# Kernel optimization log

Measured on AMD Instinct MI355X. Metric: run time of the kernel, lower is better.

## Reference

```python
import jax, jax.numpy as jnp
import numpy as np

N = 50000
E = 1600000


def _gcn_norm(edge_index, num_nodes):
    # PyG gcn_norm with add_self_loops=True, edge_weight=1:
    # append self loops, deg = in-degree over dst (col), norm = d_src^-1/2 * d_dst^-1/2
    loops = jnp.arange(num_nodes, dtype=edge_index.dtype)
    src = jnp.concatenate([edge_index[0], loops])
    dst = jnp.concatenate([edge_index[1], loops])
    deg = jax.ops.segment_sum(jnp.ones_like(dst, dtype=jnp.float32), dst,
                              num_segments=num_nodes)
    dinv = jnp.where(deg > 0, jax.lax.rsqrt(deg), 0.0)
    norm = dinv[src] * dinv[dst]  # [E+N]
    return src, dst, norm


def _gcn_layer(x, W, b, src, dst, norm, num_nodes):
    h = x @ W                                  # [N, out]
    msg = h[src] * norm[:, None]               # gather + scale, [E+N, out]
    out = jax.ops.segment_sum(msg, dst, num_segments=num_nodes)
    return out + b


def setup_inputs() -> dict:
    key = jax.random.key(0)
    ks = jax.random.split(key, 10)
    d_in, d_h, d_out = 128, 128, 64
    s = lambda d: 1.0 / np.sqrt(d)
    return {
        "x": jax.random.normal(ks[0], (N, d_in), dtype=jnp.float32),
        "edge_index": jax.random.randint(ks[1], (2, E), 0, N, dtype=jnp.int64),
        "W1": jax.random.normal(ks[2], (d_in, d_h), dtype=jnp.float32) * s(d_in),
        "b1": jnp.zeros((d_h,), dtype=jnp.float32),
        "W2": jax.random.normal(ks[3], (d_h, d_h), dtype=jnp.float32) * s(d_h),
        "b2": jnp.zeros((d_h,), dtype=jnp.float32),
        "W3": jax.random.normal(ks[4], (d_h, d_h), dtype=jnp.float32) * s(d_h),
        "b3": jnp.zeros((d_h,), dtype=jnp.float32),
        "W4": jax.random.normal(ks[5], (d_h, d_out), dtype=jnp.float32) * s(d_h),
        "b4": jnp.zeros((d_out,), dtype=jnp.float32),
    }


def reference(x, edge_index, W1, b1, W2, b2, W3, b3, W4, b4):
    src, dst, norm = _gcn_norm(edge_index, N)
    h = jax.nn.relu(_gcn_layer(x, W1, b1, src, dst, norm, N))
    h = jax.nn.relu(_gcn_layer(h, W2, b2, src, dst, norm, N))
    h = jax.nn.relu(_gcn_layer(h, W3, b3, src, dst, norm, N))
    h = _gcn_layer(h, W4, b4, src, dst, norm, N)
    return h
```

## Files before the change

kernel.cpp:

```cpp
#include <hip/hip_runtime.h>
#include <hip/hip_fp16.h>

constexpr int K_DIM = 128;

typedef short bf16x8 __attribute__((ext_vector_type(8)));
typedef float f32x4 __attribute__((ext_vector_type(4)));
typedef unsigned uint4e __attribute__((ext_vector_type(4)));

#define GLOAD16(g, l) __builtin_amdgcn_global_load_lds( \
    (const __attribute__((address_space(1))) void*)(g), \
    (__attribute__((address_space(3))) void*)(l), 16, 0, 0)

__device__ __forceinline__ unsigned short f2bf(float f) {
  unsigned u = __float_as_uint(f);
  u += 0x7fff + ((u >> 16) & 1);
  return (unsigned short)(u >> 16);
}
__device__ __forceinline__ float bf2f(unsigned short s) {
  return __uint_as_float(((unsigned)s) << 16);
}

__global__ void zerob_k(int* __restrict__ bcount, int NBr) {
  int t = threadIdx.x;
  if (t < NBr) bcount[t] = 0;
}

__global__ __launch_bounds__(256) void bcount_k(const int* __restrict__ dst, int E,
    int* __restrict__ bcount, int NBr) {
  __shared__ int h[256];
  const int tid = threadIdx.x;
  h[tid] = 0;
  __syncthreads();
  for (int t = blockIdx.x * 256 + tid; t < E; t += gridDim.x * 256)
    atomicAdd(&h[dst[t] >> 8], 1);
  __syncthreads();
  if (tid < NBr && h[tid]) atomicAdd(&bcount[tid], h[tid]);
}

__global__ __launch_bounds__(256) void bscan_k(const int* __restrict__ bcount,
    int* __restrict__ bstart, int* __restrict__ bcursor, int NBr) {
  __shared__ int sh[256];
  const int t = threadIdx.x;
  sh[t] = (t < NBr) ? bcount[t] : 0;
  __syncthreads();
  for (int off = 1; off < 256; off <<= 1) {
    int w = (t >= off) ? sh[t - off] : 0;
    __syncthreads();
    sh[t] += w;
    __syncthreads();
  }
  if (t < NBr) {
    int ex = t ? sh[t - 1] : 0;
    bstart[t] = ex;
    bcursor[t] = ex;
  }
  if (t == NBr - 1) bstart[NBr] = sh[t];
}

__global__ __launch_bounds__(256) void bscatter_k(const int* __restrict__ ei, int E,
    int* __restrict__ bcursor, unsigned* __restrict__ brec, int NBr) {
  __shared__ int h[256];
  __shared__ int base[256];
  const int tid = threadIdx.x;
  h[tid] = 0;
  __syncthreads();
  const int chunk = (E + gridDim.x - 1) / gridDim.x;
  const int s = blockIdx.x * chunk;
  const int e = min(E, s + chunk);
  for (int t = s + tid; t < e; t += 256) atomicAdd(&h[ei[E + t] >> 8], 1);
  __syncthreads();
  if (tid < NBr && h[tid]) base[tid] = atomicAdd(&bcursor[tid], h[tid]);
  __syncthreads();
  for (int t = s + tid; t < e; t += 256) {
    int src = ei[t];
    int d = ei[E + t];
    int bk = d >> 8;
    int p = atomicAdd(&base[bk], 1);
    brec[p] = ((unsigned)src << 8) | (unsigned)(d & 255);
  }
}

__global__ __launch_bounds__(256) void bcsr_k(const unsigned* __restrict__ brec,
    const int* __restrict__ bstart, int n, int E,
    int* __restrict__ rowptr, int* __restrict__ colidx, float* __restrict__ dinv) {
  __shared__ int s_deg[256];
  __shared__ int s_cur[256];
  __shared__ int s_lrp[257];
  const int b = blockIdx.x, tid = threadIdx.x;
  const int node0 = b << 8;
  const int LC = min(256, n - node0);
  const int rs = bstart[b], cnt = bstart[b + 1] - rs;

  s_deg[tid] = (tid < LC) ? 1 : 0;
  __syncthreads();
  for (int i = tid; i < cnt; i += 256) atomicAdd(&s_deg[brec[rs + i] & 255], 1);
  __syncthreads();
  s_cur[tid] = s_deg[tid];
  __syncthreads();
  for (int off = 1; off < 256; off <<= 1) {
    int w = (tid >= off) ? s_cur[tid - off] : 0;
    __syncthreads();
    s_cur[tid] += w;
    __syncthreads();
  }
  s_lrp[tid + 1] = s_cur[tid];
  if (tid == 0) s_lrp[0] = 0;
  __syncthreads();

  const int gbase = rs + node0;
  if (tid < LC) {
    int p = s_lrp[tid];
    colidx[gbase + p] = node0 + tid;
    s_cur[tid] = p + 1;
    rowptr[node0 + tid] = gbase + p;
    dinv[node0 + tid] = rsqrtf((float)(s_lrp[tid + 1] - p));
  }
  __syncthreads();
  for (int i = tid; i < cnt; i += 256) {
    unsigned r = brec[rs + i];
    int p = atomicAdd(&s_cur[r & 255], 1);
    colidx[gbase + p] = (int)(r >> 8);
  }
  if (b == (int)gridDim.x - 1 && tid == 0) rowptr[n] = E + n;
}

__global__ __launch_bounds__(256) void split_k(const float* __restrict__ x,
    unsigned* __restrict__ zh, unsigned* __restrict__ zl, long total4) {
  long t = (long)blockIdx.x * 256 + threadIdx.x;
  if (t >= total4) return;
  float4 v = reinterpret_cast<const float4*>(x)[t];
  unsigned short hx = f2bf(v.x), hy = f2bf(v.y), hz = f2bf(v.z), hw = f2bf(v.w);
  unsigned short lx = f2bf(v.x - bf2f(hx)), ly = f2bf(v.y - bf2f(hy));
  unsigned short lz = f2bf(v.z - bf2f(hz)), lw = f2bf(v.w - bf2f(hw));
  reinterpret_cast<uint2*>(zh)[t] = make_uint2((unsigned)hx | ((unsigned)hy << 16),
                                               (unsigned)hz | ((unsigned)hw << 16));
  reinterpret_cast<uint2*>(zl)[t] = make_uint2((unsigned)lx | ((unsigned)ly << 16),
                                               (unsigned)lz | ((unsigned)lw << 16));
}

__global__ __launch_bounds__(256) void wprep_k(
    const float* __restrict__ W1, const float* __restrict__ W2,
    const float* __restrict__ W3, const float* __restrict__ W4,
    unsigned short* __restrict__ wth, unsigned short* __restrict__ wtl) {
  int id = blockIdx.x * 256 + threadIdx.x;
  if (id >= 57344) return;
  const float* W;
  int nout, base, rem;
  if (id < 49152) {
    int l = id / 16384;
    W = (l == 0) ? W1 : (l == 1) ? W2 : W3;
    nout = 128;
    base = l * 16384;
    rem = id - base;
  } else {
    W = W4;
    nout = 64;
    base = 49152;
    rem = id - base;
  }
  int k = rem / nout, c = rem % nout;
  float w = W[k * nout + c];
  unsigned short hi = f2bf(w);
  unsigned short lo = f2bf(w - bf2f(hi));
  wth[base + c * 128 + k] = hi;
  wtl[base + c * 128 + k] = lo;
}

template<int NOUT>
__global__ __launch_bounds__(256) void gemm_mfma_k(
    const unsigned short* __restrict__ Zh, const unsigned short* __restrict__ Zl,
    const unsigned short* __restrict__ Wh, const unsigned short* __restrict__ Wl,
    const float* __restrict__ dinv, __half* __restrict__ H, int n) {
  constexpr int NT = NOUT / 16;
  __shared__ unsigned short Ah[64][32];
  __shared__ unsigned short Al[64][32];
  __shared__ unsigned short Bh[NOUT][32];
  __shared__ unsigned short Bl[NOUT][32];
  const int tid = threadIdx.x;
  const int lane = tid & 63;
  const int w = tid >> 6;
  const int r16 = lane & 15;
  const int kb = lane >> 4;
  const int row0 = blockIdx.x * 64;

  f32x4 acc[NT];
  #pragma unroll
  for (int t = 0; t < NT; ++t)
    #pragma unroll
    for (int q = 0; q < 4; ++q) acc[t][q] = 0.f;

  char* AhB = (char*)&Ah[0][0];
  char* AlB = (char*)&Al[0][0];
  char* BhB = (char*)&Bh[0][0];
  char* BlB = (char*)&Bl[0][0];

  for (int kc = 0; kc < 128; kc += 32) {
    __syncthreads();
    {
      int rc = row0 + (tid >> 2); rc = (rc < n) ? rc : (n - 1);
      const unsigned short* gh = Zh + (size_t)rc * 128 + kc + (tid & 3) * 8;
      const unsigned short* gl = Zl + (size_t)rc * 128 + kc + (tid & 3) * 8;
      GLOAD16(gh, AhB + w * 1024);
      GLOAD16(gl, AlB + w * 1024);
    }
    {
      const unsigned short* gh = Wh + (size_t)(tid >> 2) * 128 + kc + (tid & 3) * 8;
      const unsigned short* gl = Wl + (size_t)(tid >> 2) * 128 + kc + (tid & 3) * 8;
      GLOAD16(gh, BhB + w * 1024);
      GLOAD16(gl, BlB + w * 1024);
      if constexpr (NOUT == 128) {
        int i1 = tid + 256;
        const unsigned short* gh1 = Wh + (size_t)(i1 >> 2) * 128 + kc + (i1 & 3) * 8;
        const unsigned short* gl1 = Wl + (size_t)(i1 >> 2) * 128 + kc + (i1 & 3) * 8;
        GLOAD16(gh1, BhB + 4096 + w * 1024);
        GLOAD16(gl1, BlB + 4096 + w * 1024);
      }
    }
    __syncthreads();

    bf16x8 ah = *(const bf16x8*)&Ah[w * 16 + r16][kb * 8];
    bf16x8 al = *(const bf16x8*)&Al[w * 16 + r16][kb * 8];
    #pragma unroll
    for (int t = 0; t < NT; ++t) {
      bf16x8 bh = *(const bf16x8*)&Bh[t * 16 + r16][kb * 8];
      bf16x8 bl = *(const bf16x8*)&Bl[t * 16 + r16][kb * 8];
      acc[t] = __builtin_amdgcn_mfma_f32_16x16x32_bf16(ah, bh, acc[t], 0, 0, 0);
      acc[t] = __builtin_amdgcn_mfma_f32_16x16x32_bf16(ah, bl, acc[t], 0, 0, 0);
      acc[t] = __builtin_amdgcn_mfma_f32_16x16x32_bf16(al, bh, acc[t], 0, 0, 0);
    }
  }

  #pragma unroll
  for (int q = 0; q < 4; ++q) {
    int grow = row0 + w * 16 + kb * 4 + q;
    if (grow < n) {
      float dsc = dinv[grow];
      #pragma unroll
      for (int t = 0; t < NT; ++t)
        H[(size_t)grow * NOUT + t * 16 + r16] = __float2half(dsc * acc[t][q]);
    }
  }
}

__global__ __launch_bounds__(256) void agg128_k(const __half* __restrict__ H,
    const int* __restrict__ rowptr, const int* __restrict__ colidx,
    const float* __restrict__ dinv, const float* __restrict__ bias,
    unsigned* __restrict__ Zh, unsigned* __restrict__ Zl, int n) {
  const int wave = threadIdx.x >> 6;
  const int lane = threadIdx.x & 63;
  const int node = blockIdx.x * 4 + wave;
  if (node >= n) return;
  const int s = rowptr[node], e = rowptr[node + 1];
  const __half2* H2 = reinterpret_cast<const __half2*>(H);

  float ax = 0.f, ay = 0.f;
  for (int base = s; base < e; base += 64) {
    int m = e - base;
    int c = __builtin_nontemporal_load(&colidx[base + ((lane < m) ? lane : 0)]);
    int kmax = (m < 64) ? m : 64;
    int k = 0;
    for (; k + 7 < kmax; k += 8) {
      int cc[8];
      float2 hh[8];
      #pragma unroll
      for (int u = 0; u < 8; ++u) cc[u] = __shfl(c, k + u);
      #pragma unroll
      for (int u = 0; u < 8; ++u) hh[u] = __half22float2(H2[(size_t)cc[u] * 64 + lane]);
      #pragma unroll
      for (int u = 0; u < 8; ++u) { ax += hh[u].x; ay += hh[u].y; }
    }
    for (; k < kmax; ++k) {
      int ck = __shfl(c, k);
      float2 h = __half22float2(H2[(size_t)ck * 64 + lane]);
      ax += h.x;
      ay += h.y;
    }
  }
  float d = dinv[node];
  float2 b2 = reinterpret_cast<const float2*>(bias)[lane];
  float ox = fmaxf(fmaf(d, ax, b2.x), 0.f);
  float oy = fmaxf(fmaf(d, ay, b2.y), 0.f);
  unsigned short hx = f2bf(ox), hy = f2bf(oy);
  unsigned short lx = f2bf(ox - bf2f(hx)), ly = f2bf(oy - bf2f(hy));
  unsigned vh = (unsigned)hx | ((unsigned)hy << 16);
  unsigned vl = (unsigned)lx | ((unsigned)ly << 16);
  __builtin_nontemporal_store(vh, &Zh[(size_t)node * 64 + lane]);
  __builtin_nontemporal_store(vl, &Zl[(size_t)node * 64 + lane]);
}

__global__ __launch_bounds__(256) void agg64_k(const __half* __restrict__ H,
    const int* __restrict__ rowptr, const int* __restrict__ colidx,
    const float* __restrict__ dinv, const float* __restrict__ bias,
    float* __restrict__ out, int n) {
  const int wave = threadIdx.x >> 6;
  const int lane = threadIdx.x & 63;
  const int node = blockIdx.x * 4 + wave;
  if (node >= n) return;
  const int s = rowptr[node], e = rowptr[node + 1];

  float a0 = 0.f;
  for (int base = s; base < e; base += 64) {
    int m = e - base;
    int c = __builtin_nontemporal_load(&colidx[base + ((lane < m) ? lane : 0)]);
    int kmax = (m < 64) ? m : 64;
    int k = 0;
    for (; k + 7 < kmax; k += 8) {
      int cc[8];
      float hh[8];
      #pragma unroll
      for (int u = 0; u < 8; ++u) cc[u] = __shfl(c, k + u);
      #pragma unroll
      for (int u = 0; u < 8; ++u) hh[u] = __half2float(H[(size_t)cc[u] * 64 + lane]);
      #pragma unroll
      for (int u = 0; u < 8; ++u) a0 += hh[u];
    }
    for (; k < kmax; ++k) {
      int ck = __shfl(c, k);
      a0 += __half2float(H[(size_t)ck * 64 + lane]);
    }
  }
  float o = fmaf(dinv[node], a0, bias[lane]);
  __builtin_nontemporal_store(o, &out[(size_t)node * 64 + lane]);
}

extern "C" void kernel_launch(void* const* d_in, const int* in_sizes, int n_in,
                              void* d_out, int out_size, void* d_ws, size_t ws_size,
                              hipStream_t stream) {
  const int n = in_sizes[0] / K_DIM;
  const int E = in_sizes[1] / 2;
  const int NBr = (n + 255) >> 8;

  const float* x  = (const float*)d_in[0];
  const int*   ei = (const int*)d_in[1];
  const float* W1 = (const float*)d_in[2];
  const float* b1 = (const float*)d_in[3];
  const float* W2 = (const float*)d_in[4];
  const float* b2 = (const float*)d_in[5];
  const float* W3 = (const float*)d_in[6];
  const float* b3 = (const float*)d_in[7];
  const float* W4 = (const float*)d_in[8];
  const float* b4 = (const float*)d_in[9];
  float* out = (float*)d_out;

  char* ws = (char*)d_ws;
  size_t off = 0;
  auto alloc = [&](size_t bytes) -> void* {
    void* p = ws + off;
    off += (bytes + 255) & ~(size_t)255;
    return p;
  };
  int*      bcount  = (int*)     alloc(256 * 4);
  int*      bstart  = (int*)     alloc(257 * 4);
  int*      bcursor = (int*)     alloc(256 * 4);
  unsigned* brec    = (unsigned*)alloc((size_t)E * 4);
  int*      rowptr  = (int*)     alloc((size_t)(n + 1) * 4);
  int*      colidx  = (int*)     alloc((size_t)(E + n) * 4);
  float*    dinv    = (float*)   alloc((size_t)n * 4);
  unsigned short* Zh = (unsigned short*)alloc((size_t)n * 128 * 2);
  unsigned short* Zl = (unsigned short*)alloc((size_t)n * 128 * 2);
  __half*   hH      = (__half*)  alloc((size_t)n * 128 * 2);
  unsigned short* wth = (unsigned short*)alloc((size_t)57344 * 2);
  unsigned short* wtl = (unsigned short*)alloc((size_t)57344 * 2);

  zerob_k<<<1, 256, 0, stream>>>(bcount, NBr);
  bcount_k<<<512, 256, 0, stream>>>(ei + E, E, bcount, NBr);
  bscan_k<<<1, 256, 0, stream>>>(bcount, bstart, bcursor, NBr);
  bscatter_k<<<256, 256, 0, stream>>>(ei, E, bcursor, brec, NBr);
  bcsr_k<<<NBr, 256, 0, stream>>>(brec, bstart, n, E, rowptr, colidx, dinv);

  const long total4 = (long)n * 32;
  split_k<<<(int)((total4 + 255) / 256), 256, 0, stream>>>(x, (unsigned*)Zh, (unsigned*)Zl, total4);
  wprep_k<<<224, 256, 0, stream>>>(W1, W2, W3, W4, wth, wtl);

  const int gb = (n + 63) / 64;
  const int ab = (n + 3) / 4;

  gemm_mfma_k<128><<<gb, 256, 0, stream>>>(Zh, Zl, wth, wtl, dinv, hH, n);
  agg128_k<<<ab, 256, 0, stream>>>(hH, rowptr, colidx, dinv, b1, (unsigned*)Zh, (unsigned*)Zl, n);
  gemm_mfma_k<128><<<gb, 256, 0, stream>>>(Zh, Zl, wth + 16384, wtl + 16384, dinv, hH, n);
  agg128_k<<<ab, 256, 0, stream>>>(hH, rowptr, colidx, dinv, b2, (unsigned*)Zh, (unsigned*)Zl, n);
  gemm_mfma_k<128><<<gb, 256, 0, stream>>>(Zh, Zl, wth + 32768, wtl + 32768, dinv, hH, n);
  agg128_k<<<ab, 256, 0, stream>>>(hH, rowptr, colidx, dinv, b3, (unsigned*)Zh, (unsigned*)Zl, n);
  gemm_mfma_k<64><<<gb, 256, 0, stream>>>(Zh, Zl, wth + 49152, wtl + 49152, dinv, hH, n);
  agg64_k<<<ab, 256, 0, stream>>>(hH, rowptr, colidx, dinv, b4, out, n);
}
```

Measured before the change: 324.0 us.

## Split hidden features into column halves and restructure GEMM with register-held weights

The GEMM now keeps the W tiles in registers, loads the full 64x128 A tile into swizzled LDS once, and has each wave compute a 32-row by half-column block. For 128-wide layers it writes H as two column-major halves of 64 features. Aggregation for those layers runs as two passes, one per half, with each half-wave gathering 32 half2 values per edge, two edges at a time. The aim is a smaller gather working set per pass for better L2 hit rates, plus fewer LDS round trips and syncs in the GEMM. The cost is double the CSR traversal and launches, more register pressure, and a cross-half-wave reduction.

New measurement: 409.6 us. +26.4%, slower.

```diff
diff --git a/kernel.cpp b/kernel.cpp
--- a/kernel.cpp
+++ b/kernel.cpp
@@ -5,7 +5,6 @@
 
 typedef short bf16x8 __attribute__((ext_vector_type(8)));
 typedef float f32x4 __attribute__((ext_vector_type(4)));
-typedef unsigned uint4e __attribute__((ext_vector_type(4)));
 
 #define GLOAD16(g, l) __builtin_amdgcn_global_load_lds( \
     (const __attribute__((address_space(1))) void*)(g), \
@@ -167,91 +166,107 @@
 }
 
 template<int NOUT>
-__global__ __launch_bounds__(256) void gemm_mfma_k(
+__global__ __launch_bounds__(256, 2) void gemm_mfma_k(
     const unsigned short* __restrict__ Zh, const unsigned short* __restrict__ Zl,
     const unsigned short* __restrict__ Wh, const unsigned short* __restrict__ Wl,
     const float* __restrict__ dinv, __half* __restrict__ H, int n) {
-  constexpr int NT = NOUT / 16;
-  __shared__ unsigned short Ah[64][32];
-  __shared__ unsigned short Al[64][32];
-  __shared__ unsigned short Bh[NOUT][32];
-  __shared__ unsigned short Bl[NOUT][32];
+  constexpr int CT = NOUT / 32;
+  __shared__ unsigned short Ah[64 * 128];
+  __shared__ unsigned short Al[64 * 128];
   const int tid = threadIdx.x;
   const int lane = tid & 63;
   const int w = tid >> 6;
   const int r16 = lane & 15;
   const int kb = lane >> 4;
   const int row0 = blockIdx.x * 64;
-
-  f32x4 acc[NT];
+  const int rbase = (w & 1) * 32;
+  const int cb = (w >> 1) * (NOUT / 2);
+
+  bf16x8 bh[CT][4], bl[CT][4];
   #pragma unroll
-  for (int t = 0; t < NT; ++t)
+  for (int t = 0; t < CT; ++t)
     #pragma unroll
-    for (int q = 0; q < 4; ++q) acc[t][q] = 0.f;
-
-  char* AhB = (char*)&Ah[0][0];
-  char* AlB = (char*)&Al[0][0];
-  char* BhB = (char*)&Bh[0][0];
-  char* BlB = (char*)&Bl[0][0];
-
-  for (int kc = 0; kc < 128; kc += 32) {
-    __syncthreads();
-    {
-      int rc = row0 + (tid >> 2); rc = (rc < n) ? rc : (n - 1);
-      const unsigned short* gh = Zh + (size_t)rc * 128 + kc + (tid & 3) * 8;
-      const unsigned short* gl = Zl + (size_t)rc * 128 + kc + (tid & 3) * 8;
-      GLOAD16(gh, AhB + w * 1024);
-      GLOAD16(gl, AlB + w * 1024);
-    }
-    {
-      const unsigned short* gh = Wh + (size_t)(tid >> 2) * 128 + kc + (tid & 3) * 8;
-      const unsigned short* gl = Wl + (size_t)(tid >> 2) * 128 + kc + (tid & 3) * 8;
-      GLOAD16(gh, BhB + w * 1024);
-      GLOAD16(gl, BlB + w * 1024);
-      if constexpr (NOUT == 128) {
-        int i1 = tid + 256;
-        const unsigned short* gh1 = Wh + (size_t)(i1 >> 2) * 128 + kc + (i1 & 3) * 8;
-        const unsigned short* gl1 = Wl + (size_t)(i1 >> 2) * 128 + kc + (i1 & 3) * 8;
-        GLOAD16(gh1, BhB + 4096 + w * 1024);
-        GLOAD16(gl1, BlB + 4096 + w * 1024);
+    for (int kc = 0; kc < 4; ++kc) {
+      size_t boff = (size_t)(cb + t * 16 + r16) * 128 + kc * 32 + kb * 8;
+      bh[t][kc] = *(const bf16x8*)&Wh[boff];
+      bl[t][kc] = *(const bf16x8*)&Wl[boff];
+    }
+
+  char* AhB = (char*)Ah;
+  char* AlB = (char*)Al;
+  #pragma unroll
+  for (int it = 0; it < 4; ++it) {
+    int i = it * 256 + tid;
+    int r = i >> 4;
+    int k2 = (i & 15) ^ (r & 7);
+    int rc = row0 + r; rc = (rc < n) ? rc : (n - 1);
+    GLOAD16(Zh + (size_t)rc * 128 + k2 * 8, AhB + it * 4096 + w * 1024);
+    GLOAD16(Zl + (size_t)rc * 128 + k2 * 8, AlB + it * 4096 + w * 1024);
+  }
+  __syncthreads();
+
+  f32x4 acc[2][CT];
+  #pragma unroll
+  for (int rf = 0; rf < 2; ++rf)
+    #pragma unroll
+    for (int t = 0; t < CT; ++t)
+      #pragma unroll
+      for (int q = 0; q < 4; ++q) acc[rf][t][q] = 0.f;
+
+  const int r0 = rbase + r16;
+  const int r1 = rbase + 16 + r16;
+  const int sw = r16 & 7;
+  #pragma unroll
+  for (int kc = 0; kc < 4; ++kc) {
+    int k2s = (kc * 4 + kb) ^ sw;
+    bf16x8 ah0 = *(const bf16x8*)(AhB + r0 * 256 + k2s * 16);
+    bf16x8 al0 = *(const bf16x8*)(AlB + r0 * 256 + k2s * 16);
+    bf16x8 ah1 = *(const bf16x8*)(AhB + r1 * 256 + k2s * 16);
+    bf16x8 al1 = *(const bf16x8*)(AlB + r1 * 256 + k2s * 16);
+    #pragma unroll
+    for (int t = 0; t < CT; ++t) {
+      acc[0][t] = __builtin_amdgcn_mfma_f32_16x16x32_bf16(ah0, bh[t][kc], acc[0][t], 0, 0, 0);
+      acc[0][t] = __builtin_amdgcn_mfma_f32_16x16x32_bf16(ah0, bl[t][kc], acc[0][t], 0, 0, 0);
+      acc[0][t] = __builtin_amdgcn_mfma_f32_16x16x32_bf16(al0, bh[t][kc], acc[0][t], 0, 0, 0);
+      acc[1][t] = __builtin_amdgcn_mfma_f32_16x16x32_bf16(ah1, bh[t][kc], acc[1][t], 0, 0, 0);
+      acc[1][t] = __builtin_amdgcn_mfma_f32_16x16x32_bf16(ah1, bl[t][kc], acc[1][t], 0, 0, 0);
+      acc[1][t] = __builtin_amdgcn_mfma_f32_16x16x32_bf16(al1, bh[t][kc], acc[1][t], 0, 0, 0);
+    }
+  }
+
+  #pragma unroll
+  for (int rf = 0; rf < 2; ++rf)
+    #pragma unroll
+    for (int q = 0; q < 4; ++q) {
+      int grow = row0 + rbase + rf * 16 + kb * 4 + q;
+      if (grow < n) {
+        float dsc = dinv[grow];
+        #pragma unroll
+        for (int t = 0; t < CT; ++t) {
+          int col = cb + t * 16 + r16;
+          size_t dst;
+          if constexpr (NOUT == 128)
+            dst = (size_t)(col >> 6) * ((size_t)n * 64) + (size_t)grow * 64 + (col & 63);
+          else
+            dst = (size_t)grow * 64 + col;
+          H[dst] = __float2half(dsc * acc[rf][t][q]);
+        }
       }
     }
-    __syncthreads();
-
-    bf16x8 ah = *(const bf16x8*)&Ah[w * 16 + r16][kb * 8];
-    bf16x8 al = *(const bf16x8*)&Al[w * 16 + r16][kb * 8];
-    #pragma unroll
-    for (int t = 0; t < NT; ++t) {
-      bf16x8 bh = *(const bf16x8*)&Bh[t * 16 + r16][kb * 8];
-      bf16x8 bl = *(const bf16x8*)&Bl[t * 16 + r16][kb * 8];
-      acc[t] = __builtin_amdgcn_mfma_f32_16x16x32_bf16(ah, bh, acc[t], 0, 0, 0);
-      acc[t] = __builtin_amdgcn_mfma_f32_16x16x32_bf16(ah, bl, acc[t], 0, 0, 0);
-      acc[t] = __builtin_amdgcn_mfma_f32_16x16x32_bf16(al, bh, acc[t], 0, 0, 0);
-    }
-  }
-
-  #pragma unroll
-  for (int q = 0; q < 4; ++q) {
-    int grow = row0 + w * 16 + kb * 4 + q;
-    if (grow < n) {
-      float dsc = dinv[grow];
-      #pragma unroll
-      for (int t = 0; t < NT; ++t)
-        H[(size_t)grow * NOUT + t * 16 + r16] = __float2half(dsc * acc[t][q]);
-    }
-  }
-}
-
-__global__ __launch_bounds__(256) void agg128_k(const __half* __restrict__ H,
+}
+
+__global__ __launch_bounds__(256) void agg128h_k(const __half* __restrict__ Hh,
     const int* __restrict__ rowptr, const int* __restrict__ colidx,
     const float* __restrict__ dinv, const float* __restrict__ bias,
-    unsigned* __restrict__ Zh, unsigned* __restrict__ Zl, int n) {
+    unsigned short* __restrict__ Zhd, unsigned short* __restrict__ Zld, int n) {
   const int wave = threadIdx.x >> 6;
   const int lane = threadIdx.x & 63;
   const int node = blockIdx.x * 4 + wave;
   if (node >= n) return;
+  const int l31 = lane & 31;
+  const int g = lane >> 5;
   const int s = rowptr[node], e = rowptr[node + 1];
-  const __half2* H2 = reinterpret_cast<const __half2*>(H);
+  const __half2* H2 = reinterpret_cast<const __half2*>(Hh);
 
   float ax = 0.f, ay = 0.f;
   for (int base = s; base < e; base += 64) {
@@ -259,33 +274,38 @@
     int c = __builtin_nontemporal_load(&colidx[base + ((lane < m) ? lane : 0)]);
     int kmax = (m < 64) ? m : 64;
     int k = 0;
-    for (; k + 7 < kmax; k += 8) {
-      int cc[8];
-      float2 hh[8];
-      #pragma unroll
-      for (int u = 0; u < 8; ++u) cc[u] = __shfl(c, k + u);
-      #pragma unroll
-      for (int u = 0; u < 8; ++u) hh[u] = __half22float2(H2[(size_t)cc[u] * 64 + lane]);
+    for (; k + 15 < kmax; k += 16) {
+      int cc[8]; float2 hh[8];
+      #pragma unroll
+      for (int u = 0; u < 8; ++u) cc[u] = __shfl(c, k + 2 * u + g);
+      #pragma unroll
+      for (int u = 0; u < 8; ++u) hh[u] = __half22float2(H2[(size_t)cc[u] * 32 + l31]);
       #pragma unroll
       for (int u = 0; u < 8; ++u) { ax += hh[u].x; ay += hh[u].y; }
     }
-    for (; k < kmax; ++k) {
-      int ck = __shfl(c, k);
-      float2 h = __half22float2(H2[(size_t)ck * 64 + lane]);
-      ax += h.x;
-      ay += h.y;
-    }
-  }
-  float d = dinv[node];
-  float2 b2 = reinterpret_cast<const float2*>(bias)[lane];
-  float ox = fmaxf(fmaf(d, ax, b2.x), 0.f);
-  float oy = fmaxf(fmaf(d, ay, b2.y), 0.f);
-  unsigned short hx = f2bf(ox), hy = f2bf(oy);
-  unsigned short lx = f2bf(ox - bf2f(hx)), ly = f2bf(oy - bf2f(hy));
-  unsigned vh = (unsigned)hx | ((unsigned)hy << 16);
-  unsigned vl = (unsigned)lx | ((unsigned)ly << 16);
-  __builtin_nontemporal_store(vh, &Zh[(size_t)node * 64 + lane]);
-  __builtin_nontemporal_store(vl, &Zl[(size_t)node * 64 + lane]);
+    for (; k < kmax; k += 2) {
+      int kk = k + g;
+      int ck = __shfl(c, (kk < kmax) ? kk : k);
+      if (kk < kmax) {
+        float2 hv = __half22float2(H2[(size_t)ck * 32 + l31]);
+        ax += hv.x; ay += hv.y;
+      }
+    }
+  }
+  ax += __shfl_xor(ax, 32);
+  ay += __shfl_xor(ay, 32);
+  if (g == 0) {
+    float d = dinv[node];
+    float2 b2 = reinterpret_cast<const float2*>(bias)[l31];
+    float ox = fmaxf(fmaf(d, ax, b2.x), 0.f);
+    float oy = fmaxf(fmaf(d, ay, b2.y), 0.f);
+    unsigned short hx = f2bf(ox), hy = f2bf(oy);
+    unsigned short lx = f2bf(ox - bf2f(hx)), ly = f2bf(oy - bf2f(hy));
+    unsigned vh = (unsigned)hx | ((unsigned)hy << 16);
+    unsigned vl = (unsigned)lx | ((unsigned)ly << 16);
+    __builtin_nontemporal_store(vh, (unsigned*)(Zhd + (size_t)node * 128) + l31);
+    __builtin_nontemporal_store(vl, (unsigned*)(Zld + (size_t)node * 128) + l31);
+  }
 }
 
 __global__ __launch_bounds__(256) void agg64_k(const __half* __restrict__ H,
@@ -375,12 +395,18 @@
   const int gb = (n + 63) / 64;
   const int ab = (n + 3) / 4;
 
-  gemm_mfma_k<128><<<gb, 256, 0, stream>>>(Zh, Zl, wth, wtl, dinv, hH, n);
-  agg128_k<<<ab, 256, 0, stream>>>(hH, rowptr, colidx, dinv, b1, (unsigned*)Zh, (unsigned*)Zl, n);
-  gemm_mfma_k<128><<<gb, 256, 0, stream>>>(Zh, Zl, wth + 16384, wtl + 16384, dinv, hH, n);
-  agg128_k<<<ab, 256, 0, stream>>>(hH, rowptr, colidx, dinv, b2, (unsigned*)Zh, (unsigned*)Zl, n);
-  gemm_mfma_k<128><<<gb, 256, 0, stream>>>(Zh, Zl, wth + 32768, wtl + 32768, dinv, hH, n);
-  agg128_k<<<ab, 256, 0, stream>>>(hH, rowptr, colidx, dinv, b3, (unsigned*)Zh, (unsigned*)Zl, n);
+  const float* biases[3] = {b1, b2, b3};
+  const unsigned short* wh[3] = {wth, wth + 16384, wth + 32768};
+  const unsigned short* wl[3] = {wtl, wtl + 16384, wtl + 32768};
+
+  for (int l = 0; l < 3; ++l) {
+    gemm_mfma_k<128><<<gb, 256, 0, stream>>>(Zh, Zl, wh[l], wl[l], dinv, hH, n);
+    for (int h = 0; h < 2; ++h) {
+      agg128h_k<<<ab, 256, 0, stream>>>(hH + (size_t)h * n * 64, rowptr, colidx,
+                                        dinv, biases[l] + h * 64,
+                                        Zh + h * 64, Zl + h * 64, n);
+    }
+  }
   gemm_mfma_k<64><<<gb, 256, 0, stream>>>(Zh, Zl, wth + 49152, wtl + 49152, dinv, hH, n);
   agg64_k<<<ab, 256, 0, stream>>>(hH, rowptr, colidx, dinv, b4, out, n);
 }
```
